# Performance work log

Hardware: AMD Instinct MI355X
Metric: run time of the kernel (lower is better)

The kernel has to match this reference:

```python
import jax, jax.numpy as jnp
import numpy as np
from jax import lax

B, N, G, K = 32, 8192, 512, 32
CH = [64, 128, 256]
EPS = 1e-5


def setup_inputs() -> dict:
    key = jax.random.key(0)
    ks = jax.random.split(key, 8)
    inp = {"points": jax.random.normal(ks[0], (B, N, 3), dtype=jnp.float32)}
    last = 3
    for li, c in enumerate(CH):
        inp[f"w{li}"] = jax.random.normal(ks[li + 1], (c, last), jnp.float32) * (1.0 / np.sqrt(last))
        inp[f"b{li}"] = jnp.zeros((c,), jnp.float32)
        inp[f"gamma{li}"] = jnp.ones((c,), jnp.float32)
        inp[f"beta{li}"] = jnp.zeros((c,), jnp.float32)
        inp[f"mean{li}"] = jnp.zeros((c,), jnp.float32)
        inp[f"var{li}"] = jnp.ones((c,), jnp.float32)
        last = c
    return inp


def _fps(xyz, npoint):
    # farthest point sampling: xyz [B,N,3] -> indices [B, npoint]
    b, n, _ = xyz.shape
    first = jnp.zeros((b,), jnp.int32)

    def step(carry, _):
        mindist, last_idx = carry
        last = jnp.take_along_axis(xyz, last_idx[:, None, None], axis=1)  # [B,1,3]
        d = jnp.sum((xyz - last) ** 2, axis=-1)  # [B,N]
        mindist = jnp.minimum(mindist, d)
        nxt = jnp.argmax(mindist, axis=-1).astype(jnp.int32)
        return (mindist, nxt), nxt

    init = (jnp.full((b, n), 1e10, jnp.float32), first)
    _, rest = lax.scan(step, init, None, length=npoint - 1)  # [npoint-1, B]
    return jnp.concatenate([first[None, :], rest], axis=0).T  # [B, npoint]


def _sample_and_group(points):
    idx_c = _fps(points, G)                                           # [B,G]
    centers = jnp.take_along_axis(points, idx_c[..., None], axis=1)   # [B,G,3]
    # kNN: squared distance [B,G,N]
    d = jnp.sum((centers[:, :, None, :] - points[:, None, :, :]) ** 2, axis=-1)
    _, idx = lax.top_k(-d, K)                                         # [B,G,K]
    grouped = jax.vmap(lambda p, i: p[i])(points, idx)                # [B,G,K,3]
    neighborhoods = grouped - centers[:, :, None, :]                  # recenter
    return neighborhoods, centers


def _mlp_maxpool(neigh, layers):
    h = neigh  # [B,G,K,C]
    for (w, b, g, be, m, v) in layers:
        h = jnp.einsum('bgkc,oc->bgko', h, w) + b       # 1x1 conv == linear
        h = (h - m) * (g / jnp.sqrt(v + EPS)) + be      # BatchNorm (inference)
        h = jax.nn.relu(h)
    return jnp.max(h, axis=(1, 2))                      # max over K then G == max over both


def reference(points, w0, b0, gamma0, beta0, mean0, var0,
              w1, b1, gamma1, beta1, mean1, var1,
              w2, b2, gamma2, beta2, mean2, var2):
    neigh, _ = _sample_and_group(points)
    layers = [(w0, b0, gamma0, beta0, mean0, var0),
              (w1, b1, gamma1, beta1, mean1, var1),
              (w2, b2, gamma2, beta2, mean2, var2)]
    return _mlp_maxpool(neigh, layers)  # [B, 256]
```

## Files before the change

### kernel.cpp

```cpp
#include <hip/hip_runtime.h>

#define B_ 32
#define N_ 8192
#define G_ 512
#define K_ 32
#define EPSF 1e-5f

typedef __attribute__((ext_vector_type(8))) short bf16x8;
typedef __attribute__((ext_vector_type(4))) float f32x4;
typedef __attribute__((ext_vector_type(2))) unsigned long long u64x2;

static __device__ __forceinline__ short f2bf(float f) {
    unsigned u = __float_as_uint(f);
    u += 0x7fffu + ((u >> 16) & 1u);
    return (short)(u >> 16);
}

static __device__ __forceinline__ unsigned long long u64max(unsigned long long a,
                                                            unsigned long long b) {
    return a > b ? a : b;
}
static __device__ __forceinline__ unsigned long long u64min(unsigned long long a,
                                                            unsigned long long b) {
    return a < b ? a : b;
}

template <int CTL>
static __device__ __forceinline__ unsigned long long dpp_shr_u64(unsigned long long k) {
    const int lo = __builtin_amdgcn_mov_dpp((int)(unsigned)k, CTL, 0xf, 0xf, true);
    const int hi = __builtin_amdgcn_mov_dpp((int)(unsigned)(k >> 32), CTL, 0xf, 0xf, true);
    return ((unsigned long long)(unsigned)hi << 32) | (unsigned)lo;
}

template <int CTL>
static __device__ __forceinline__ unsigned long long dpp_upd_u64(unsigned long long k) {
    const int lo = __builtin_amdgcn_update_dpp((int)(unsigned)k, (int)(unsigned)k,
                                               CTL, 0xf, 0xf, false);
    const int hi = __builtin_amdgcn_update_dpp((int)(unsigned)(k >> 32),
                                               (int)(unsigned)(k >> 32),
                                               CTL, 0xf, 0xf, false);
    return ((unsigned long long)(unsigned)hi << 32) | (unsigned)lo;
}

__global__ __launch_bounds__(256) void prep_kernel(
    const float* __restrict__ w0, const float* __restrict__ b0,
    const float* __restrict__ g0, const float* __restrict__ be0,
    const float* __restrict__ m0, const float* __restrict__ v0,
    const float* __restrict__ w1, const float* __restrict__ b1,
    const float* __restrict__ g1, const float* __restrict__ be1,
    const float* __restrict__ m1, const float* __restrict__ v1,
    const float* __restrict__ w2, const float* __restrict__ b2,
    const float* __restrict__ g2, const float* __restrict__ be2,
    const float* __restrict__ m2, const float* __restrict__ v2,
    float* __restrict__ W0b, float* __restrict__ b1b, float* __restrict__ b2b,
    short* __restrict__ W1b, short* __restrict__ W2b) {
    const int t = threadIdx.x;
    if (t < 64) {
        const float sc = g0[t] / sqrtf(v0[t] + EPSF);
        W0b[t * 4 + 0] = w0[t * 3 + 0] * sc;
        W0b[t * 4 + 1] = w0[t * 3 + 1] * sc;
        W0b[t * 4 + 2] = w0[t * 3 + 2] * sc;
        W0b[t * 4 + 3] = (b0[t] - m0[t]) * sc + be0[t];
    }
    if (t < 128) b1b[t] = (b1[t] - m1[t]) * (g1[t] / sqrtf(v1[t] + EPSF)) + be1[t];
    if (t < 256) b2b[t] = (b2[t] - m2[t]) * (g2[t] / sqrtf(v2[t] + EPSF)) + be2[t];
    for (int i = t; i < 128 * 64; i += 256) {
        const int o = i >> 6;
        const float sc = g1[o] / sqrtf(v1[o] + EPSF);
        W1b[i] = f2bf(w1[i] * sc);
    }
    for (int i = t; i < 256 * 128; i += 256) {
        const int o = i >> 7;
        const float sc = g2[o] / sqrtf(v2[o] + EPSF);
        W2b[i] = f2bf(w2[i] * sc);
    }
}

__global__ __launch_bounds__(512) void fps_kernel(const float* __restrict__ pts,
                                                  float* __restrict__ centers) {
    __shared__ float4 sxyz[N_];
    __shared__ __align__(16) unsigned long long rowkeys[2][32];

    const int b = blockIdx.x;
    const int t = threadIdx.x;
    const int l = t & 63;
    const int w = t >> 6;
    const float* p = pts + (size_t)b * (N_ * 3);

    float px[16], py[16], pz[16], md[16];
#pragma unroll
    for (int j = 0; j < 16; ++j) {
        const int idx = t + j * 512;
        px[j] = p[3 * idx + 0];
        py[j] = p[3 * idx + 1];
        pz[j] = p[3 * idx + 2];
        sxyz[idx] = make_float4(px[j], py[j], pz[j], 0.0f);
        md[j] = 1e10f;
    }
    __syncthreads();

    if (t == 0) {
        float* c = centers + (size_t)b * (G_ * 3);
        c[0] = px[0]; c[1] = py[0]; c[2] = pz[0];
    }
    float4 c0 = sxyz[0];
    float lx = c0.x, ly = c0.y, lz = c0.z;
    const int pay0 = 8191 - t;

    for (int g = 1; g < G_; ++g) {
        float m_best = -1.0f;
        int j_best = 0;
#pragma unroll
        for (int j = 0; j < 16; ++j) {
            const float dx = __fsub_rn(px[j], lx);
            const float dy = __fsub_rn(py[j], ly);
            const float dz = __fsub_rn(pz[j], lz);
            const float d = __fadd_rn(__fadd_rn(__fmul_rn(dx, dx), __fmul_rn(dy, dy)),
                                      __fmul_rn(dz, dz));
            const float m = fminf(md[j], d);
            md[j] = m;
            const bool c = m > m_best;
            m_best = c ? m : m_best;
            j_best = c ? j : j_best;
        }
        unsigned long long key =
            ((unsigned long long)__float_as_uint(m_best) << 13) |
            (unsigned long long)(unsigned)(pay0 - (j_best << 9));

        key = u64max(key, dpp_shr_u64<0x111>(key));
        key = u64max(key, dpp_shr_u64<0x112>(key));
        key = u64max(key, dpp_shr_u64<0x114>(key));
        key = u64max(key, dpp_shr_u64<0x118>(key));
        if ((l & 15) == 15) rowkeys[g & 1][w * 4 + (l >> 4)] = key;
        __syncthreads();

        const u64x2* rk = (const u64x2*)&rowkeys[g & 1][0];
        const u64x2 k2 = rk[l & 15];
        unsigned long long kk = u64max(k2[0], k2[1]);
        kk = u64max(kk, dpp_shr_u64<0x111>(kk));
        kk = u64max(kk, dpp_shr_u64<0x112>(kk));
        kk = u64max(kk, dpp_shr_u64<0x114>(kk));
        kk = u64max(kk, dpp_shr_u64<0x118>(kk));
        const unsigned blo =
            (unsigned)__builtin_amdgcn_readlane((int)(unsigned)kk, 15);
        const int last = 8191 - (int)(blo & 0x1FFFu);

        const float4 cc = sxyz[last];
        lx = cc.x; ly = cc.y; lz = cc.z;
        if (t == 0) {
            float* c = centers + ((size_t)b * G_ + g) * 3;
            c[0] = lx; c[1] = ly; c[2] = lz;
        }
    }
}

__global__ __launch_bounds__(256) void knn_kernel(const float* __restrict__ pts,
                                                  const float* __restrict__ centers,
                                                  float* __restrict__ neigh) {
    __shared__ unsigned long long wkeys[4][32];
    __shared__ int midx[32];

    const int cid = blockIdx.x;
    const int b = cid >> 9;
    const int t = threadIdx.x;
    const int w = t >> 6;
    const int l = t & 63;
    const float* p = pts + (size_t)b * (N_ * 3);
    const float* c = centers + (size_t)cid * 3;
    const float cx = c[0], cy = c[1], cz = c[2];

    const int iy0 = (w << 11) + l;

    unsigned int db[32];
#pragma unroll
    for (int i = 0; i < 32; ++i) {
        const int idx = iy0 + (i << 6);
        const float dx = __fsub_rn(p[3 * idx + 0], cx);
        const float dy = __fsub_rn(p[3 * idx + 1], cy);
        const float dz = __fsub_rn(p[3 * idx + 2], cz);
        const float d = __fadd_rn(__fadd_rn(__fmul_rn(dx, dx), __fmul_rn(dy, dy)),
                                  __fmul_rn(dz, dz));
        db[i] = __float_as_uint(d);
    }

    unsigned int excl = 0u;
    unsigned long long gm0, gm1, gm2, gm3;

#define KNN_SCAN_GROUP(G, DEST)                                               \
    {                                                                         \
        unsigned long long nm = ~0ull;                                        \
        _Pragma("unroll") for (int j = 0; j < 8; ++j) {                       \
            const int i = ((G) << 3) + j;                                     \
            if (!(excl & (1u << i))) {                                        \
                const unsigned long long k2 =                                 \
                    ((unsigned long long)db[i] << 13) |                       \
                    (unsigned long long)(unsigned)(iy0 + (i << 6));           \
                nm = (nm < k2) ? nm : k2;                                     \
            }                                                                 \
        }                                                                     \
        DEST = nm;                                                            \
    }

    KNN_SCAN_GROUP(0, gm0)
    KNN_SCAN_GROUP(1, gm1)
    KNN_SCAN_GROUP(2, gm2)
    KNN_SCAN_GROUP(3, gm3)
    unsigned long long lkey = u64min(u64min(gm0, gm1), u64min(gm2, gm3));

    for (int r = 0; r < K_; ++r) {
        unsigned long long x = lkey;
        x = u64min(x, dpp_upd_u64<0x111>(x));
        x = u64min(x, dpp_upd_u64<0x112>(x));
        x = u64min(x, dpp_upd_u64<0x114>(x));
        x = u64min(x, dpp_upd_u64<0x118>(x));
        x = u64min(x, dpp_upd_u64<0x142>(x));
        x = u64min(x, dpp_upd_u64<0x143>(x));
        const unsigned blo = (unsigned)__builtin_amdgcn_readlane((int)(unsigned)x, 63);
        const unsigned bhi =
            (unsigned)__builtin_amdgcn_readlane((int)(unsigned)(x >> 32), 63);
        const unsigned long long best = ((unsigned long long)bhi << 32) | blo;

        if (best == lkey) {
            const int i = ((int)(best & 0x1FFFull) >> 6) & 31;
            excl |= 1u << i;
            switch (i >> 3) {
                case 0: KNN_SCAN_GROUP(0, gm0) break;
                case 1: KNN_SCAN_GROUP(1, gm1) break;
                case 2: KNN_SCAN_GROUP(2, gm2) break;
                default: KNN_SCAN_GROUP(3, gm3) break;
            }
            lkey = u64min(u64min(gm0, gm1), u64min(gm2, gm3));
        }
        if (l == 0) wkeys[w][r] = best;
    }
#undef KNN_SCAN_GROUP
    __syncthreads();

    if (t < 128) {
        const int wv = t >> 5;
        const int pos = t & 31;
        const unsigned long long mykey = wkeys[wv][pos];
        int rank = pos;
#pragma unroll
        for (int d = 1; d < 4; ++d) {
            const int ol = (wv + d) & 3;
            int cnt = 0;
#pragma unroll
            for (int s = 32; s >= 1; s >>= 1) {
                const int n = cnt + s;
                if (n <= 32 && wkeys[ol][n - 1] < mykey) cnt = n;
            }
            rank += cnt;
        }
        if (rank < 32) midx[rank] = (int)(mykey & 0x1FFFull);
    }
    __syncthreads();

    if (t < 32) {
        const int idx = midx[t];
        float* o3 = neigh + (((size_t)cid * K_) + t) * 3;
        o3[0] = __fsub_rn(p[3 * idx + 0], cx);
        o3[1] = __fsub_rn(p[3 * idx + 1], cy);
        o3[2] = __fsub_rn(p[3 * idx + 2], cz);
    }
}

__global__ __launch_bounds__(512) void mlp_kernel(
    const float* __restrict__ neigh, const float* __restrict__ W0b,
    const float* __restrict__ b1b, const float* __restrict__ b2b,
    const short* __restrict__ W1b, const short* __restrict__ W2b,
    float* __restrict__ out) {
    __shared__ bf16x8 lw1v[1024];
    __shared__ bf16x8 lw2v[4096];
    __shared__ bf16x8 lh2v[8 * 512];
    __shared__ float lw0[256];
    __shared__ float lb1[128];
    __shared__ float lb2[256];
    __shared__ float colmax[256];

    const int t = threadIdx.x;
    const int w = t >> 6;
    const int l = t & 63;
    const int lr = l & 15;
    const int lg = l >> 4;

    {
        char* d1 = (char*)lw1v;
        for (int i = t; i < 1024; i += 512) {
            const int d = i * 16;
            const int src = d ^ ((((unsigned)d >> 7) & 7) << 4);
            *(bf16x8*)(d1 + d) = *(const bf16x8*)((const char*)W1b + src);
        }
        char* d2 = (char*)lw2v;
        for (int i = t; i < 4096; i += 512) {
            const int d = i * 16;
            const int src = d ^ ((((unsigned)d >> 8) & 7) << 4);
            *(bf16x8*)(d2 + d) = *(const bf16x8*)((const char*)W2b + src);
        }
        if (t < 256) lw0[t] = W0b[t];
        if (t < 128) lb1[t] = b1b[t];
        if (t < 256) lb2[t] = b2b[t];
        if (t < 256) colmax[t] = 0.0f;
    }
    __syncthreads();

    const size_t pbase = (size_t)blockIdx.x * 256 + w * 32;
    bf16x8 a1[2][2];
#pragma unroll
    for (int m = 0; m < 2; ++m) {
        const float* pp = neigh + (pbase + m * 16 + lr) * 3;
        const float x0 = pp[0], x1 = pp[1], x2 = pp[2];
#pragma unroll
        for (int s = 0; s < 2; ++s) {
            bf16x8 v;
#pragma unroll
            for (int j = 0; j < 8; ++j) {
                const int c = s * 32 + lg * 8 + j;
                const float4 wv = *(const float4*)&lw0[c * 4];
                float val = fmaf(x2, wv.z, fmaf(x1, wv.y, x0 * wv.x)) + wv.w;
                v[j] = f2bf(fmaxf(val, 0.0f));
            }
            a1[m][s] = v;
        }
    }

    const f32x4 vzero = {0.f, 0.f, 0.f, 0.f};
    f32x4 acc2[2][8];
#pragma unroll
    for (int m = 0; m < 2; ++m)
#pragma unroll
        for (int n = 0; n < 8; ++n) acc2[m][n] = vzero;

    const char* w1p = (const char*)lw1v;
#pragma unroll
    for (int s = 0; s < 2; ++s) {
#pragma unroll
        for (int n = 0; n < 8; ++n) {
            const int o = n * 16 + lr;
            int byte = o * 128 + s * 64 + lg * 16;
            byte ^= ((o & 7) << 4);
            const bf16x8 bfr = *(const bf16x8*)(w1p + byte);
            acc2[0][n] = __builtin_amdgcn_mfma_f32_16x16x32_bf16(a1[0][s], bfr, acc2[0][n], 0, 0, 0);
            acc2[1][n] = __builtin_amdgcn_mfma_f32_16x16x32_bf16(a1[1][s], bfr, acc2[1][n], 0, 0, 0);
        }
    }

    char* myh2 = (char*)(lh2v + w * 512);
#pragma unroll
    for (int m = 0; m < 2; ++m)
#pragma unroll
        for (int n = 0; n < 8; ++n) {
            const int o = n * 16 + lr;
            const float bb = lb1[o];
#pragma unroll
            for (int q = 0; q < 4; ++q) {
                const int row = m * 16 + lg * 4 + q;
                int byte = row * 256 + o * 2;
                byte ^= ((row & 7) << 4);
                *(short*)(myh2 + byte) = f2bf(fmaxf(acc2[m][n][q] + bb, 0.0f));
            }
        }

    f32x4 acc3[2][16];
#pragma unroll
    for (int m = 0; m < 2; ++m)
#pragma unroll
        for (int n = 0; n < 16; ++n) acc3[m][n] = vzero;

    const char* w2p = (const char*)lw2v;
#pragma unroll
    for (int s = 0; s < 4; ++s) {
        bf16x8 a[2];
#pragma unroll
        for (int m = 0; m < 2; ++m) {
            const int row = m * 16 + lr;
            int byte = row * 256 + s * 64 + lg * 16;
            byte ^= ((row & 7) << 4);
            a[m] = *(const bf16x8*)(myh2 + byte);
        }
#pragma unroll
        for (int n = 0; n < 16; ++n) {
            const int o = n * 16 + lr;
            int byte = o * 256 + s * 64 + lg * 16;
            byte ^= ((o & 7) << 4);
            const bf16x8 bfr = *(const bf16x8*)(w2p + byte);
            acc3[0][n] = __builtin_amdgcn_mfma_f32_16x16x32_bf16(a[0], bfr, acc3[0][n], 0, 0, 0);
            acc3[1][n] = __builtin_amdgcn_mfma_f32_16x16x32_bf16(a[1], bfr, acc3[1][n], 0, 0, 0);
        }
    }

#pragma unroll
    for (int n = 0; n < 16; ++n) {
        const int o = n * 16 + lr;
        const float bb = lb2[o];
        float mx = 0.0f;
#pragma unroll
        for (int m = 0; m < 2; ++m)
#pragma unroll
            for (int q = 0; q < 4; ++q) mx = fmaxf(mx, acc3[m][n][q] + bb);
        mx = fmaxf(mx, 0.0f);
        mx = fmaxf(mx, __shfl_xor(mx, 16, 64));
        mx = fmaxf(mx, __shfl_xor(mx, 32, 64));
        if (lg == 0) atomicMax((unsigned int*)&colmax[o], __float_as_uint(mx));
    }
    __syncthreads();
    if (t < 256) {
        const int b = (int)(blockIdx.x >> 6);
        atomicMax((unsigned int*)out + b * 256 + t, __float_as_uint(colmax[t]));
    }
}

extern "C" void kernel_launch(void* const* d_in, const int* in_sizes, int n_in,
                              void* d_out, int out_size, void* d_ws, size_t ws_size,
                              hipStream_t stream) {
    const float* pts = (const float*)d_in[0];
    const float* w0 = (const float*)d_in[1];
    const float* b0 = (const float*)d_in[2];
    const float* g0 = (const float*)d_in[3];
    const float* be0 = (const float*)d_in[4];
    const float* m0 = (const float*)d_in[5];
    const float* v0 = (const float*)d_in[6];
    const float* w1 = (const float*)d_in[7];
    const float* b1 = (const float*)d_in[8];
    const float* g1 = (const float*)d_in[9];
    const float* be1 = (const float*)d_in[10];
    const float* m1 = (const float*)d_in[11];
    const float* v1 = (const float*)d_in[12];
    const float* w2 = (const float*)d_in[13];
    const float* b2 = (const float*)d_in[14];
    const float* g2 = (const float*)d_in[15];
    const float* be2 = (const float*)d_in[16];
    const float* m2 = (const float*)d_in[17];
    const float* v2 = (const float*)d_in[18];

    char* ws = (char*)d_ws;
    float* centers = (float*)ws;
    float* neigh = (float*)(ws + (size_t)262144);
    char* wb = ws + (size_t)6553600;
    float* W0b = (float*)(wb + 0);
    float* b1b = (float*)(wb + 1024);
    float* b2b = (float*)(wb + 1536);
    short* W1b = (short*)(wb + 2560);
    short* W2b = (short*)(wb + 2560 + 16384);

    hipMemsetAsync(d_out, 0, (size_t)out_size * sizeof(float), stream);
    prep_kernel<<<1, 256, 0, stream>>>(w0, b0, g0, be0, m0, v0,
                                       w1, b1, g1, be1, m1, v1,
                                       w2, b2, g2, be2, m2, v2,
                                       W0b, b1b, b2b, W1b, W2b);
    fps_kernel<<<B_, 512, 0, stream>>>(pts, centers);
    knn_kernel<<<B_ * G_, 256, 0, stream>>>(pts, centers, neigh);
    mlp_kernel<<<(B_ * G_ * K_) / 256, 512, 0, stream>>>(
        neigh, W0b, b1b, b2b, W1b, W2b, (float*)d_out);
}
```

Measured before the change: 928.4 us.

## Restructure FPS argmax into 32-bit value max plus winner atomic coordinate broadcast

The farthest-point-sampling loop now first reduces only the 32-bit distance value, using a register tree, DPP row shifts, row broadcasts and one LDS atomicMax per wave. Threads holding the maximum then atomicMin packed (index, coordinate) keys, so the winner's xyz is broadcast directly. This removes the 64-bit key DPP passes, the LDS point copy and the per-iteration centre stores, which are instead collected in registers and written once at the end. The cost is an extra barrier per iteration plus atomics, and tie-breaking has to stay equivalent to the reference's lowest-index argmax.

```diff
diff --git a/kernel.cpp b/kernel.cpp
--- a/kernel.cpp
+++ b/kernel.cpp
@@ -16,20 +16,17 @@
     return (short)(u >> 16);
 }
 
-static __device__ __forceinline__ unsigned long long u64max(unsigned long long a,
-                                                            unsigned long long b) {
-    return a > b ? a : b;
-}
 static __device__ __forceinline__ unsigned long long u64min(unsigned long long a,
                                                             unsigned long long b) {
     return a < b ? a : b;
 }
+static __device__ __forceinline__ unsigned umax32(unsigned a, unsigned b) {
+    return a > b ? a : b;
+}
 
 template <int CTL>
-static __device__ __forceinline__ unsigned long long dpp_shr_u64(unsigned long long k) {
-    const int lo = __builtin_amdgcn_mov_dpp((int)(unsigned)k, CTL, 0xf, 0xf, true);
-    const int hi = __builtin_amdgcn_mov_dpp((int)(unsigned)(k >> 32), CTL, 0xf, 0xf, true);
-    return ((unsigned long long)(unsigned)hi << 32) | (unsigned)lo;
+static __device__ __forceinline__ unsigned dpp_mov_u32(unsigned v) {
+    return (unsigned)__builtin_amdgcn_mov_dpp((int)v, CTL, 0xf, 0xf, true);
 }
 
 template <int CTL>
@@ -78,13 +75,13 @@
 
 __global__ __launch_bounds__(512) void fps_kernel(const float* __restrict__ pts,
                                                   float* __restrict__ centers) {
-    __shared__ float4 sxyz[N_];
-    __shared__ __align__(16) unsigned long long rowkeys[2][32];
+    __shared__ unsigned mslot[2];
+    __shared__ unsigned long long kslot[2][3];
+    __shared__ float4 c0s;
 
     const int b = blockIdx.x;
     const int t = threadIdx.x;
     const int l = t & 63;
-    const int w = t >> 6;
     const float* p = pts + (size_t)b * (N_ * 3);
 
     float px[16], py[16], pz[16], md[16];
@@ -94,22 +91,22 @@
         px[j] = p[3 * idx + 0];
         py[j] = p[3 * idx + 1];
         pz[j] = p[3 * idx + 2];
-        sxyz[idx] = make_float4(px[j], py[j], pz[j], 0.0f);
         md[j] = 1e10f;
     }
-    __syncthreads();
-
+    if (t < 2) mslot[t] = 0u;
+    if (t < 6) kslot[t / 3][t % 3] = ~0ull;
+
+    float k0x = 0.f, k0y = 0.f, k0z = 0.f, k1x = 0.f, k1y = 0.f, k1z = 0.f;
     if (t == 0) {
         float* c = centers + (size_t)b * (G_ * 3);
         c[0] = px[0]; c[1] = py[0]; c[2] = pz[0];
-    }
-    float4 c0 = sxyz[0];
-    float lx = c0.x, ly = c0.y, lz = c0.z;
-    const int pay0 = 8191 - t;
+        c0s = make_float4(px[0], py[0], pz[0], 0.f);
+        k0x = px[0]; k0y = py[0]; k0z = pz[0];
+    }
+    __syncthreads();
+    float lx = c0s.x, ly = c0s.y, lz = c0s.z;
 
     for (int g = 1; g < G_; ++g) {
-        float m_best = -1.0f;
-        int j_best = 0;
 #pragma unroll
         for (int j = 0; j < 16; ++j) {
             const float dx = __fsub_rn(px[j], lx);
@@ -117,40 +114,70 @@
             const float dz = __fsub_rn(pz[j], lz);
             const float d = __fadd_rn(__fadd_rn(__fmul_rn(dx, dx), __fmul_rn(dy, dy)),
                                       __fmul_rn(dz, dz));
-            const float m = fminf(md[j], d);
-            md[j] = m;
-            const bool c = m > m_best;
-            m_best = c ? m : m_best;
-            j_best = c ? j : j_best;
-        }
-        unsigned long long key =
-            ((unsigned long long)__float_as_uint(m_best) << 13) |
-            (unsigned long long)(unsigned)(pay0 - (j_best << 9));
-
-        key = u64max(key, dpp_shr_u64<0x111>(key));
-        key = u64max(key, dpp_shr_u64<0x112>(key));
-        key = u64max(key, dpp_shr_u64<0x114>(key));
-        key = u64max(key, dpp_shr_u64<0x118>(key));
-        if ((l & 15) == 15) rowkeys[g & 1][w * 4 + (l >> 4)] = key;
+            md[j] = fminf(md[j], d);
+        }
+        float tv[16];
+#pragma unroll
+        for (int j = 0; j < 16; ++j) tv[j] = md[j];
+#pragma unroll
+        for (int s = 8; s >= 1; s >>= 1)
+#pragma unroll
+            for (int k = 0; k < s; ++k) tv[k] = fmaxf(tv[k], tv[k + s]);
+        const unsigned vbits = __float_as_uint(tv[0]);
+
+        unsigned vv = vbits;
+        vv = umax32(vv, dpp_mov_u32<0x111>(vv));
+        vv = umax32(vv, dpp_mov_u32<0x112>(vv));
+        vv = umax32(vv, dpp_mov_u32<0x114>(vv));
+        vv = umax32(vv, dpp_mov_u32<0x118>(vv));
+        vv = umax32(vv, dpp_mov_u32<0x142>(vv));
+        vv = umax32(vv, dpp_mov_u32<0x143>(vv));
+        if (l == 63) atomicMax(&mslot[g & 1], vv);
         __syncthreads();
 
-        const u64x2* rk = (const u64x2*)&rowkeys[g & 1][0];
-        const u64x2 k2 = rk[l & 15];
-        unsigned long long kk = u64max(k2[0], k2[1]);
-        kk = u64max(kk, dpp_shr_u64<0x111>(kk));
-        kk = u64max(kk, dpp_shr_u64<0x112>(kk));
-        kk = u64max(kk, dpp_shr_u64<0x114>(kk));
-        kk = u64max(kk, dpp_shr_u64<0x118>(kk));
-        const unsigned blo =
-            (unsigned)__builtin_amdgcn_readlane((int)(unsigned)kk, 15);
-        const int last = 8191 - (int)(blo & 0x1FFFu);
-
-        const float4 cc = sxyz[last];
-        lx = cc.x; ly = cc.y; lz = cc.z;
-        if (t == 0) {
-            float* c = centers + ((size_t)b * G_ + g) * 3;
-            c[0] = lx; c[1] = ly; c[2] = lz;
-        }
+        const unsigned mstar = mslot[g & 1];
+
+        if (t == 0) mslot[(g + 1) & 1] = 0u;
+        if (t < 3) kslot[(g + 1) & 1][t] = ~0ull;
+
+        if (vbits == mstar) {
+            int jb = 15;
+            float wx_ = px[15], wy_ = py[15], wz_ = pz[15];
+#pragma unroll
+            for (int j = 14; j >= 0; --j) {
+                const bool c = (__float_as_uint(md[j]) == mstar);
+                jb = c ? j : jb;
+                wx_ = c ? px[j] : wx_;
+                wy_ = c ? py[j] : wy_;
+                wz_ = c ? pz[j] : wz_;
+            }
+            const unsigned long long kb =
+                ((unsigned long long)(unsigned)((jb << 9) | t)) << 32;
+            atomicMin(&kslot[g & 1][0], kb | (unsigned long long)__float_as_uint(wx_));
+            atomicMin(&kslot[g & 1][1], kb | (unsigned long long)__float_as_uint(wy_));
+            atomicMin(&kslot[g & 1][2], kb | (unsigned long long)__float_as_uint(wz_));
+        }
+        __syncthreads();
+
+        lx = __uint_as_float((unsigned)kslot[g & 1][0]);
+        ly = __uint_as_float((unsigned)kslot[g & 1][1]);
+        lz = __uint_as_float((unsigned)kslot[g & 1][2]);
+
+        const bool cap = (t == (g & 255));
+        const bool hi = g >= 256;
+        k0x = (cap && !hi) ? lx : k0x;
+        k0y = (cap && !hi) ? ly : k0y;
+        k0z = (cap && !hi) ? lz : k0z;
+        k1x = (cap && hi) ? lx : k1x;
+        k1y = (cap && hi) ? ly : k1y;
+        k1z = (cap && hi) ? lz : k1z;
+    }
+
+    if (t < 256) {
+        float* c = centers + ((size_t)b * G_ + t) * 3;
+        c[0] = k0x; c[1] = k0y; c[2] = k0z;
+        float* c2 = centers + ((size_t)b * G_ + 256 + t) * 3;
+        c2[0] = k1x; c2[1] = k1y; c2[2] = k1z;
     }
 }
 
```

Measured after the change: 1.101 ms. 1.19x slower.
